# Kernel optimization log

Measured on AMD Instinct MI355X. Metric: run time of the kernel, lower is better.

The kernel has to match this reference:

```python
import jax, jax.numpy as jnp
import numpy as np

B, S, DIM, FF = 64, 577, 768, 3072
BLK = 8          # block_shape = (8, 8)
DENSITY = 0.1    # fraction of 8x8 blocks that are nonzero


def _expand_block_mask(m):
    # m: [out//BLK, in//BLK] bool -> [out, in] float mask
    return jnp.repeat(jnp.repeat(m, BLK, axis=0), BLK, axis=1)


def setup_inputs() -> dict:
    key = jax.random.key(0)
    ks = jax.random.split(key, 7)
    x = jax.random.normal(ks[0], (B, S, DIM), dtype=jnp.float32)
    # nn.Linear-style init scale
    W1 = jax.random.normal(ks[1], (FF, DIM), dtype=jnp.float32) / np.sqrt(DIM).astype(np.float32)
    b1 = jax.random.normal(ks[2], (FF,), dtype=jnp.float32) * 0.02
    W2 = jax.random.normal(ks[3], (DIM, FF), dtype=jnp.float32) / np.sqrt(FF).astype(np.float32)
    b2 = jax.random.normal(ks[4], (DIM,), dtype=jnp.float32) * 0.02
    mask1 = jax.random.uniform(ks[5], (FF // BLK, DIM // BLK)) < DENSITY
    mask2 = jax.random.uniform(ks[6], (DIM // BLK, FF // BLK)) < DENSITY
    return {"x": x, "W1": W1, "b1": b1, "W2": W2, "b2": b2,
            "mask1": mask1, "mask2": mask2}


def reference(x, W1, b1, W2, b2, mask1, mask2):
    # fc1: block-sparse linear  y = x @ (W1 * M1)^T + b1
    Wm1 = W1 * _expand_block_mask(mask1).astype(W1.dtype)  # [FF, DIM]
    h = jnp.einsum('bsd,fd->bsf', x, Wm1) + b1             # [B, S, FF]
    h = jax.nn.gelu(h, approximate=False)                  # F.gelu default (exact)
    # fc2: block-sparse linear
    Wm2 = W2 * _expand_block_mask(mask2).astype(W2.dtype)  # [DIM, FF]
    return jnp.einsum('bsf,df->bsd', h, Wm2) + b2          # [B, S, DIM]
```

## Files before the change

### kernel.cpp

```cpp
#include <hip/hip_runtime.h>
#include <hip/hip_bf16.h>


typedef __attribute__((ext_vector_type(8))) short short8;
typedef __attribute__((ext_vector_type(16))) float f32x16;
typedef unsigned long long u64;
typedef unsigned short ushort_t;

#define DIM 768
#define FF 3072
#define NF32 96
#define NG32 24
#define NDB 96
#define NFB 384
#define MR 32
#define NT 768
#define XP 776
#define HP 1544
#define SACCP 772

#define S1CAP (NF32 * 96 + 32)
#define S2CAP (NG32 * 2 * 192 + 32)
#define W1S_TOT (S1CAP * 256)
#define W2S_TOT (S2CAP * 256)

#define MFMA32 __builtin_amdgcn_mfma_f32_32x32x16_bf16

__device__ __forceinline__ float gelu_fast(float v) {
    float t2 = v * fmaf(v * v, -0.10295667f, -2.30235629f);
    return v / (1.0f + exp2f(t2));
}
__device__ __forceinline__ ushort_t f2bs(float f) {
    union { __hip_bfloat16 h; ushort_t u; } cv;
    cv.h = __float2bfloat16(f);
    return cv.u;
}

__global__ __launch_bounds__(64)
void prep_count(const int* __restrict__ mask1, const int* __restrict__ mask2,
                int* __restrict__ cnt1, int* __restrict__ cnt2)
{
    const int l = threadIdx.x;
    const int g = blockIdx.x;
    if (g < NF32) {
        const int* r0 = mask1 + (4 * g) * NDB;
        bool ua = (r0[l] | r0[NDB + l] | r0[2 * NDB + l] | r0[3 * NDB + l]) != 0;
        u64 ba = __ballot(ua);
        bool ub = (l < 32) &&
            ((r0[64 + l] | r0[NDB + 64 + l] | r0[2 * NDB + 64 + l] | r0[3 * NDB + 64 + l]) != 0);
        u64 bb = __ballot(ub);
        if (l == 0) cnt1[g] = ((__popcll(ba) + __popcll(bb)) + 15) & ~15;
    } else {
        const int G = g - NF32;
        const int* r0 = mask2 + (4 * G) * NFB;
        int c0 = 0, c1 = 0;
        #pragma unroll
        for (int p = 0; p < 6; ++p) {
            int fb = p * 64 + l;
            u64 b = __ballot((r0[fb] | r0[NFB + fb] | r0[2 * NFB + fb] | r0[3 * NFB + fb]) != 0);
            if (p < 3) c0 += __popcll(b); else c1 += __popcll(b);
        }
        if (l == 0) {
            cnt2[0 * NG32 + G] = (c0 + 15) & ~15;
            cnt2[1 * NG32 + G] = (c1 + 15) & ~15;
        }
    }
}

__global__ __launch_bounds__(128)
void prep_scan(const int* __restrict__ cnt1, const int* __restrict__ cnt2,
               int* __restrict__ off1p, int* __restrict__ off2p,
               int* __restrict__ base1, int* __restrict__ base2,
               unsigned* __restrict__ idx1s, unsigned* __restrict__ idx2s)
{
    __shared__ int s1[97], s2[49];
    const int tid = threadIdx.x;
    if (tid < 96) s1[tid + 1] = cnt1[tid];
    if (tid < 48) s2[tid + 1] = cnt2[tid];
    __syncthreads();
    if (tid == 0) { s1[0] = 0; for (int i = 0; i < 96; ++i) s1[i + 1] += s1[i]; }
    if (tid == 1) { s2[0] = 0; for (int i = 0; i < 48; ++i) s2[i + 1] += s2[i]; }
    __syncthreads();
    if (tid < 97) off1p[tid] = s1[tid];
    if (tid < 96) base1[tid] = s1[tid];
    if (tid < 49) off2p[tid] = s2[tid];
    if (tid < 48) base2[tid] = s2[tid];
    if (tid >= 64 && tid < 96) idx1s[s1[96] + (tid - 64)] = 0;
    if (tid >= 96 && tid < 128) idx2s[s2[48] + (tid - 96)] = 0;
}

__global__ __launch_bounds__(256)
void prep_gather(const float* __restrict__ W1, const float* __restrict__ W2,
                 const int* __restrict__ mask1, const int* __restrict__ mask2,
                 const int* __restrict__ base1, const int* __restrict__ base2,
                 const int* __restrict__ cnt1, const int* __restrict__ cnt2,
                 __hip_bfloat16* __restrict__ w1s, __hip_bfloat16* __restrict__ w2s,
                 unsigned* __restrict__ idx1s, unsigned* __restrict__ idx2s)
{
    __shared__ ushort_t sidx[192];
    __shared__ int sc[1];
    const int tid = threadIdx.x;
    const int l = tid & 63;
    const int g = blockIdx.x;

    if (g < NF32) {
        const int F = g;
        const int* r0 = mask1 + (4 * F) * NDB;
        if (tid < 64) {
            bool ua = (r0[l] | r0[NDB + l] | r0[2 * NDB + l] | r0[3 * NDB + l]) != 0;
            u64 ba = __ballot(ua);
            bool ub = (l < 32) &&
                ((r0[64 + l] | r0[NDB + 64 + l] | r0[2 * NDB + 64 + l] | r0[3 * NDB + 64 + l]) != 0);
            u64 bb = __ballot(ub);
            int ca = __popcll(ba);
            if (ua) sidx[__popcll(ba & ((1ull << l) - 1ull))] = (ushort_t)l;
            if (ub) sidx[ca + __popcll(bb & ((1ull << l) - 1ull))] = (ushort_t)(64 + l);
            int cnt = ca + __popcll(bb);
            if (l == 0) {
                sc[0] = cnt;
                int cntp = (cnt + 15) & ~15;
                for (int i = cnt; i < cntp && i < 192; ++i) sidx[i] = 0;
            }
        }
        __syncthreads();
        const int cnt = sc[0];
        const int base = base1[F];
        const int cntp = cnt1[F];
        if (tid < cntp) idx1s[base + tid] = (unsigned)sidx[tid] * 8u;
        for (int e = tid; e < cntp * 256; e += 256) {
            int slot = e >> 8, c = (e >> 3) & 31, j = e & 7;
            int db = sidx[slot];
            float w = 0.f;
            if (slot < cnt && mask1[(4 * F + (c >> 3)) * NDB + db])
                w = W1[(long)(F * 32 + c) * DIM + db * 8 + j];
            w1s[(long)(base + slot) * 256 + c * 8 + j] = __float2bfloat16(w);
        }
    } else {
        const int gi = g - NF32;
        const int c = gi / NG32;
        const int G = gi % NG32;
        const int* r0 = mask2 + (4 * G) * NFB;
        if (tid < 64) {
            u64 b[3]; int pc[3];
            #pragma unroll
            for (int p = 0; p < 3; ++p) {
                int fb = c * 192 + p * 64 + l;
                b[p] = __ballot((r0[fb] | r0[NFB + fb] | r0[2 * NFB + fb] | r0[3 * NFB + fb]) != 0);
                pc[p] = __popcll(b[p]);
            }
            int basea = 0;
            #pragma unroll
            for (int p = 0; p < 3; ++p) {
                if ((b[p] >> l) & 1ull)
                    sidx[basea + __popcll(b[p] & ((1ull << l) - 1ull))] = (ushort_t)(p * 64 + l);
                basea += pc[p];
            }
            if (l == 0) {
                int cnt = basea;
                sc[0] = cnt;
                int cntp = (cnt + 15) & ~15;
                for (int i = cnt; i < cntp && i < 192; ++i) sidx[i] = 0;
            }
        }
        __syncthreads();
        const int cnt = sc[0];
        const int base = base2[c * NG32 + G];
        const int cntp = cnt2[c * NG32 + G];
        if (tid < cntp) idx2s[base + tid] = (unsigned)sidx[tid] * 8u;
        for (int e = tid; e < cntp * 256; e += 256) {
            int slot = e >> 8, cc = (e >> 3) & 31, j = e & 7;
            int lfb = sidx[slot];
            int fb = c * 192 + lfb;
            float w = 0.f;
            if (slot < cnt && mask2[(4 * G + (cc >> 3)) * NFB + fb])
                w = W2[(long)(G * 32 + cc) * FF + fb * 8 + j];
            w2s[(long)(base + slot) * 256 + cc * 8 + j] = __float2bfloat16(w);
        }
    }
}

#define PREF(BUF, IP, WP, ARR, ROWOFF)                                  \
    {                                                                   \
        uint4 qa = *(const uint4*)(IP);                                 \
        uint4 qb = *(const uint4*)((IP) + 4);                           \
        int m0 = lh ? (int)qa.y : (int)qa.x;                            \
        int m1 = lh ? (int)qa.w : (int)qa.z;                            \
        int m2 = lh ? (int)qb.y : (int)qb.x;                            \
        int m3 = lh ? (int)qb.w : (int)qb.z;                            \
        BUF##a0 = *(const short8*)&ARR[(ROWOFF) + m0];                  \
        BUF##a1 = *(const short8*)&ARR[(ROWOFF) + m1];                  \
        BUF##a2 = *(const short8*)&ARR[(ROWOFF) + m2];                  \
        BUF##a3 = *(const short8*)&ARR[(ROWOFF) + m3];                  \
        BUF##w0 = *(const short8*)(WP);                                 \
        BUF##w1 = *(const short8*)((WP) + 512);                         \
        BUF##w2 = *(const short8*)((WP) + 1024);                        \
        BUF##w3 = *(const short8*)((WP) + 1536);                        \
    }

#define PAIRSTEP(IP, WP, ARR, ROWOFF)                                   \
    {                                                                   \
        short8 a0 = Aa0, a1 = Aa1, a2 = Aa2, a3 = Aa3;                  \
        short8 w0 = Aw0, w1 = Aw1, w2 = Aw2, w3 = Aw3;                  \
        PREF(A, IP, WP, ARR, ROWOFF)                                    \
        ca = MFMA32(a0, w0, ca, 0, 0, 0);                               \
        ca = MFMA32(a1, w1, ca, 0, 0, 0);                               \
        ca = MFMA32(a2, w2, ca, 0, 0, 0);                               \
        ca = MFMA32(a3, w3, ca, 0, 0, 0);                               \
    }                                                                   \
    {                                                                   \
        short8 a0 = Ba0, a1 = Ba1, a2 = Ba2, a3 = Ba3;                  \
        short8 w0 = Bw0, w1 = Bw1, w2 = Bw2, w3 = Bw3;                  \
        PREF(B, (IP) + 8, (WP) + 2048, ARR, ROWOFF)                     \
        cb = MFMA32(a0, w0, cb, 0, 0, 0);                               \
        cb = MFMA32(a1, w1, cb, 0, 0, 0);                               \
        cb = MFMA32(a2, w2, cb, 0, 0, 0);                               \
        cb = MFMA32(a3, w3, cb, 0, 0, 0);                               \
    }                                                                   \
    IP += 16; WP += 4096; s += 16;

__global__ __launch_bounds__(NT, 3)
void bsffn_main(const float* __restrict__ x,
                const float* __restrict__ pb1, const float* __restrict__ pb2,
                const ushort_t* __restrict__ w1s, const ushort_t* __restrict__ w2s,
                const unsigned* __restrict__ idx1s, const unsigned* __restrict__ idx2s,
                const int* __restrict__ off1p, const int* __restrict__ off2p,
                float* __restrict__ out)
{
    __shared__ __align__(16) ushort_t xs[MR * XP];
    __shared__ __align__(16) ushort_t hs[MR * HP];

    const int tid = threadIdx.x;
    const int wave = tid >> 6;
    const int l = tid & 63;
    const int l31 = l & 31;
    const int lh = l >> 5;
    const int xrow = l31 * XP;
    const int hrow = l31 * HP;
    const int wlofs = lh * 256 + l31 * 8;
    const long rowBase = (long)blockIdx.x * MR;

    {
        const float* xr = x + rowBase * DIM;
        #pragma unroll
        for (int i = 0; i < 4; ++i) {
            int e = tid + i * NT;
            int row = e / 96, c8 = e % 96;
            const float4 v0 = *(const float4*)(xr + row * DIM + c8 * 8);
            const float4 v1 = *(const float4*)(xr + row * DIM + c8 * 8 + 4);
            uint4 wv;
            wv.x = (unsigned)f2bs(v0.x) | ((unsigned)f2bs(v0.y) << 16);
            wv.y = (unsigned)f2bs(v0.z) | ((unsigned)f2bs(v0.w) << 16);
            wv.z = (unsigned)f2bs(v1.x) | ((unsigned)f2bs(v1.y) << 16);
            wv.w = (unsigned)f2bs(v1.z) | ((unsigned)f2bs(v1.w) << 16);
            *(uint4*)&xs[row * XP + c8 * 8] = wv;
        }
    }

    f32x16 accA, accB;
    #pragma unroll
    for (int r = 0; r < 16; ++r) { accA[r] = 0.f; accB[r] = 0.f; }

    __syncthreads();

    for (int chunk = 0; chunk < 2; ++chunk) {
        {
            const int Fbeg = chunk * 48 + wave * 4;
            int s = off1p[Fbeg];
            const unsigned* ip = idx1s + s;
            const ushort_t* wp = w1s + (long)s * 256 + wlofs;
            short8 Aa0, Aa1, Aa2, Aa3, Aw0, Aw1, Aw2, Aw3;
            short8 Ba0, Ba1, Ba2, Ba3, Bw0, Bw1, Bw2, Bw3;
            PREF(A, ip, wp, xs, xrow)
            PREF(B, ip + 8, wp + 2048, xs, xrow)
            ip += 16; wp += 4096;
            #pragma unroll 1
            for (int j = 0; j < 4; ++j) {
                const int F = Fbeg + j;
                const int gend = off1p[F + 1];
                f32x16 ca, cb;
                #pragma unroll
                for (int r = 0; r < 16; ++r) { ca[r] = 0.f; cb[r] = 0.f; }
                while (s < gend) { PAIRSTEP(ip, wp, xs, xrow) }
                const float bias = pb1[F * 32 + l31];
                const int hcol = (F - chunk * 48) * 32 + l31;
                #pragma unroll
                for (int r = 0; r < 16; ++r) {
                    int rs = (r & 3) + 8 * (r >> 2) + 4 * lh;
                    hs[rs * HP + hcol] = f2bs(gelu_fast(ca[r] + cb[r] + bias));
                }
            }
        }
        __syncthreads();

        {
            const int k0 = chunk * 24 + wave * 2;
            int s = off2p[k0];
            const unsigned* ip = idx2s + s;
            const ushort_t* wp = w2s + (long)s * 256 + wlofs;
            short8 Aa0, Aa1, Aa2, Aa3, Aw0, Aw1, Aw2, Aw3;
            short8 Ba0, Ba1, Ba2, Ba3, Bw0, Bw1, Bw2, Bw3;
            PREF(A, ip, wp, hs, hrow)
            PREF(B, ip + 8, wp + 2048, hs, hrow)
            ip += 16; wp += 4096;
            {
                const int gend = off2p[k0 + 1];
                f32x16 ca = accA, cb;
                #pragma unroll
                for (int r = 0; r < 16; ++r) cb[r] = 0.f;
                while (s < gend) { PAIRSTEP(ip, wp, hs, hrow) }
                #pragma unroll
                for (int r = 0; r < 16; ++r) accA[r] = ca[r] + cb[r];
            }
            {
                const int gend = off2p[k0 + 2];
                f32x16 ca = accB, cb;
                #pragma unroll
                for (int r = 0; r < 16; ++r) cb[r] = 0.f;
                while (s < gend) { PAIRSTEP(ip, wp, hs, hrow) }
                #pragma unroll
                for (int r = 0; r < 16; ++r) accB[r] = ca[r] + cb[r];
            }
        }
        __syncthreads();
    }

    float* sacc = (float*)hs;
    {
        const int d0 = (wave * 2) * 32 + l31;
        const int d1 = (wave * 2 + 1) * 32 + l31;
        #pragma unroll
        for (int r = 0; r < 16; ++r) {
            int rs = (r & 3) + 8 * (r >> 2) + 4 * lh;
            sacc[rs * SACCP + d0] = accA[r];
            sacc[rs * SACCP + d1] = accB[r];
        }
    }
    __syncthreads();
    {
        const float4* pb24 = (const float4*)pb2;
        #pragma unroll
        for (int i = 0; i < 8; ++i) {
            int e = tid + i * NT;
            int row = e / 192, c4 = e % 192;
            float4 v = *(const float4*)&sacc[row * SACCP + c4 * 4];
            float4 b = pb24[c4];
            v.x += b.x; v.y += b.y; v.z += b.z; v.w += b.w;
            *(float4*)&out[(rowBase + row) * DIM + c4 * 4] = v;
        }
    }
}

extern "C" void kernel_launch(void* const* d_in, const int* in_sizes, int n_in,
                              void* d_out, int out_size, void* d_ws, size_t ws_size,
                              hipStream_t stream) {
    const float* x = (const float*)d_in[0];
    const float* W1 = (const float*)d_in[1];
    const float* b1 = (const float*)d_in[2];
    const float* W2 = (const float*)d_in[3];
    const float* b2 = (const float*)d_in[4];
    const int* mask1 = (const int*)d_in[5];
    const int* mask2 = (const int*)d_in[6];
    float* out = (float*)d_out;

    ushort_t* w1s = (ushort_t*)d_ws;
    ushort_t* w2s = w1s + W1S_TOT;
    unsigned* idx1s = (unsigned*)(w2s + W2S_TOT);
    unsigned* idx2s = idx1s + S1CAP;
    int* cnt1 = (int*)(idx2s + S2CAP);
    int* cnt2 = cnt1 + NF32;
    int* off1p = cnt2 + 2 * NG32;
    int* off2p = off1p + (NF32 + 1);
    int* base1 = off2p + (2 * NG32 + 1);
    int* base2 = base1 + NF32;

    prep_count<<<NF32 + NG32, 64, 0, stream>>>(mask1, mask2, cnt1, cnt2);
    prep_scan<<<1, 128, 0, stream>>>(cnt1, cnt2, off1p, off2p, base1, base2,
                                     idx1s, idx2s);
    prep_gather<<<NF32 + 2 * NG32, 256, 0, stream>>>(
        W1, W2, mask1, mask2, base1, base2, cnt1, cnt2,
        (__hip_bfloat16*)w1s, (__hip_bfloat16*)w2s, idx1s, idx2s);

    const int rows = in_sizes[0] / DIM;
    const int nblk = rows / MR;
    bsffn_main<<<nblk, NT, 0, stream>>>(
        x, b1, b2, w1s, w2s, idx1s, idx2s, off1p, off2p, out);
}
```

Baseline: 361.0 us.

## Use 16 waves per block and rebalance fc2 output groups across waves

Raises the main kernel's block from 12 to 16 waves. Each wave now handles 3 fc1 column groups instead of 4. In fc2, the 24 output groups are split so that the first 8 waves take two groups and the other 8 take one, with the prefix-scan order of w2 segments permuted to match. The aim is more parallelism and more waves to hide latency per block. In exchange, the occupancy hint of 3 blocks per CU is dropped, the fc2 load across waves is uneven, and register pressure per block rises.

```diff
diff --git a/kernel.cpp b/kernel.cpp
--- a/kernel.cpp
+++ b/kernel.cpp
@@ -14,7 +14,7 @@
 #define NDB 96
 #define NFB 384
 #define MR 32
-#define NT 768
+#define NT 1024
 #define XP 776
 #define HP 1544
 #define SACCP 772
@@ -25,6 +25,10 @@
 #define W2S_TOT (S2CAP * 256)
 
 #define MFMA32 __builtin_amdgcn_mfma_f32_32x32x16_bf16
+
+__host__ __device__ __forceinline__ int p2g(int p) {
+    return (p < 16) ? ((p & 1) ? 16 + (p >> 1) : (p >> 1)) : (p - 8);
+}
 
 __device__ __forceinline__ float gelu_fast(float v) {
     float t2 = v * fmaf(v * v, -0.10295667f, -2.30235629f);
@@ -73,18 +77,27 @@
                int* __restrict__ base1, int* __restrict__ base2,
                unsigned* __restrict__ idx1s, unsigned* __restrict__ idx2s)
 {
-    __shared__ int s1[97], s2[49];
+    __shared__ int s1[97], s2[49], sc2[48], sb2[48];
     const int tid = threadIdx.x;
     if (tid < 96) s1[tid + 1] = cnt1[tid];
-    if (tid < 48) s2[tid + 1] = cnt2[tid];
+    if (tid < 48) sc2[tid] = cnt2[tid];
     __syncthreads();
     if (tid == 0) { s1[0] = 0; for (int i = 0; i < 96; ++i) s1[i + 1] += s1[i]; }
-    if (tid == 1) { s2[0] = 0; for (int i = 0; i < 48; ++i) s2[i + 1] += s2[i]; }
+    if (tid == 1) {
+        s2[0] = 0;
+        for (int c = 0; c < 2; ++c)
+            for (int p = 0; p < 24; ++p) {
+                int pos = c * 24 + p;
+                int G = p2g(p);
+                s2[pos + 1] = s2[pos] + sc2[c * 24 + G];
+                sb2[c * 24 + G] = s2[pos];
+            }
+    }
     __syncthreads();
     if (tid < 97) off1p[tid] = s1[tid];
     if (tid < 96) base1[tid] = s1[tid];
     if (tid < 49) off2p[tid] = s2[tid];
-    if (tid < 48) base2[tid] = s2[tid];
+    if (tid < 48) base2[tid] = sb2[tid];
     if (tid >= 64 && tid < 96) idx1s[s1[96] + (tid - 64)] = 0;
     if (tid >= 96 && tid < 128) idx2s[s2[48] + (tid - 96)] = 0;
 }
@@ -218,7 +231,7 @@
     }                                                                   \
     IP += 16; WP += 4096; s += 16;
 
-__global__ __launch_bounds__(NT, 3)
+__global__ __launch_bounds__(NT)
 void bsffn_main(const float* __restrict__ x,
                 const float* __restrict__ pb1, const float* __restrict__ pb2,
                 const ushort_t* __restrict__ w1s, const ushort_t* __restrict__ w2s,
@@ -242,7 +255,7 @@
     {
         const float* xr = x + rowBase * DIM;
         #pragma unroll
-        for (int i = 0; i < 4; ++i) {
+        for (int i = 0; i < 3; ++i) {
             int e = tid + i * NT;
             int row = e / 96, c8 = e % 96;
             const float4 v0 = *(const float4*)(xr + row * DIM + c8 * 8);
@@ -262,9 +275,13 @@
 
     __syncthreads();
 
+    const int pos0 = (wave < 8) ? 2 * wave : wave + 8;
+    const int G0 = wave;
+    const int G1 = 16 + wave;
+
     for (int chunk = 0; chunk < 2; ++chunk) {
         {
-            const int Fbeg = chunk * 48 + wave * 4;
+            const int Fbeg = chunk * 48 + wave * 3;
             int s = off1p[Fbeg];
             const unsigned* ip = idx1s + s;
             const ushort_t* wp = w1s + (long)s * 256 + wlofs;
@@ -274,7 +291,7 @@
             PREF(B, ip + 8, wp + 2048, xs, xrow)
             ip += 16; wp += 4096;
             #pragma unroll 1
-            for (int j = 0; j < 4; ++j) {
+            for (int j = 0; j < 3; ++j) {
                 const int F = Fbeg + j;
                 const int gend = off1p[F + 1];
                 f32x16 ca, cb;
@@ -293,7 +310,7 @@
         __syncthreads();
 
         {
-            const int k0 = chunk * 24 + wave * 2;
+            const int k0 = chunk * 24 + pos0;
             int s = off2p[k0];
             const unsigned* ip = idx2s + s;
             const ushort_t* wp = w2s + (long)s * 256 + wlofs;
@@ -311,7 +328,7 @@
                 #pragma unroll
                 for (int r = 0; r < 16; ++r) accA[r] = ca[r] + cb[r];
             }
-            {
+            if (wave < 8) {
                 const int gend = off2p[k0 + 2];
                 f32x16 ca = accB, cb;
                 #pragma unroll
@@ -326,20 +343,26 @@
 
     float* sacc = (float*)hs;
     {
-        const int d0 = (wave * 2) * 32 + l31;
-        const int d1 = (wave * 2 + 1) * 32 + l31;
+        const int d0 = G0 * 32 + l31;
         #pragma unroll
         for (int r = 0; r < 16; ++r) {
             int rs = (r & 3) + 8 * (r >> 2) + 4 * lh;
             sacc[rs * SACCP + d0] = accA[r];
-            sacc[rs * SACCP + d1] = accB[r];
+        }
+        if (wave < 8) {
+            const int d1 = G1 * 32 + l31;
+            #pragma unroll
+            for (int r = 0; r < 16; ++r) {
+                int rs = (r & 3) + 8 * (r >> 2) + 4 * lh;
+                sacc[rs * SACCP + d1] = accB[r];
+            }
         }
     }
     __syncthreads();
     {
         const float4* pb24 = (const float4*)pb2;
         #pragma unroll
-        for (int i = 0; i < 8; ++i) {
+        for (int i = 0; i < 6; ++i) {
             int e = tid + i * NT;
             int row = e / 192, c4 = e % 192;
             float4 v = *(const float4*)&sacc[row * SACCP + c4 * 4];
```

New measurement: 742.8 us. +105.7%, slower.
